# Optimization experiments

Hardware: AMD Instinct MI355X
Metric: run time of the kernel (lower is better)

Reference implementation:

```python
import jax, jax.numpy as jnp
import numpy as np

B, N, F_IN, T = 4, 512, 64, 16
K, F_CHEB, F_TIME, TS = 3, 64, 64, 1
E = 16384
LN_EPS = 1e-5


def setup_inputs() -> dict:
    key = jax.random.key(0)
    ks = jax.random.split(key, 18)
    s = 0.05
    X = jax.random.normal(ks[0], (B, N, F_IN, T), jnp.float32)
    # edges with guaranteed no self-loops (so remove_self_loops is a no-op)
    src = jax.random.randint(ks[1], (E,), 0, N, jnp.int32)
    off = jax.random.randint(ks[2], (E,), 1, N, jnp.int32)
    dst = (src + off) % N
    edge_index = jnp.stack([src, dst])
    return {
        'X': X,
        'edge_index': edge_index,
        'U1': jax.random.uniform(ks[3], (N,)) * s,
        'U2': jax.random.normal(ks[4], (F_IN, N)) * s,
        'U3': jax.random.uniform(ks[5], (F_IN,)) * s,
        'be': jax.random.normal(ks[6], (1, T, T)) * s,
        'Ve': jax.random.normal(ks[7], (T, T)) * s,
        'Ws1': jax.random.uniform(ks[8], (T,)) * s,
        'Ws2': jax.random.normal(ks[9], (F_IN, T)) * s,
        'Ws3': jax.random.uniform(ks[10], (F_IN,)) * s,
        'bs': jax.random.normal(ks[11], (1, N, N)) * s,
        'Vs': jax.random.normal(ks[12], (N, N)) * s,
        'W_cheb': jax.random.normal(ks[13], (K, F_IN, F_CHEB)) * s,
        'b_cheb': jax.random.uniform(ks[14], (F_CHEB,)) * s,
        'Wt': jax.random.normal(ks[15], (F_TIME, F_CHEB, 1, 3)) * s,
        'bt': jnp.zeros((F_TIME,), jnp.float32),
        'Wr': jax.random.normal(ks[16], (F_TIME, F_IN, 1, 1)) * s,
        'br': jnp.zeros((F_TIME,), jnp.float32),
        'gamma': jnp.ones((F_TIME,), jnp.float32),
        'beta': jnp.zeros((F_TIME,), jnp.float32),
    }


def _forward(edge_index, X, U1, U2, U3, be, Ve, Ws1, Ws2, Ws3, bs, Vs,
             W_cheb, b_cheb, Wt, bt, Wr, br, gamma, beta):
    Bn, Nn, Fn, Tn = X.shape
    # ---- temporal attention: (B,T,T)
    lhs_t = jnp.einsum('bnft,n->btf', X, U1) @ U2            # (B,T,N)
    rhs_t = jnp.einsum('f,bnft->bnt', U3, X)                 # (B,N,T)
    Et = jnp.matmul(Ve, jax.nn.sigmoid(jnp.matmul(lhs_t, rhs_t) + be))
    Et = jax.nn.softmax(Et, axis=1)
    # temporally re-weighted signal
    Xt = jnp.matmul(X.reshape(Bn, Nn * Fn, Tn), Et).reshape(Bn, Nn, Fn, Tn)
    # ---- spatial attention: (B,N,N)
    lhs_s = jnp.einsum('bnft,t->bnf', Xt, Ws1) @ Ws2         # (B,N,T)
    rhs_s = jnp.einsum('f,bnft->btn', Ws3, Xt)               # (B,T,N)
    S = jnp.matmul(Vs, jax.nn.sigmoid(jnp.matmul(lhs_s, rhs_s) + bs))
    S = jax.nn.softmax(S, axis=1)                            # (B,N,N)
    # ---- scaled sym-normalized Laplacian; lambda_max=2 so 2/lambda_max = 1.
    # edges: -D^-1/2 A D^-1/2 (E), +I self loops (N), then add_self_loops(-1) (N)
    row, col = edge_index[0], edge_index[1]
    ew = jnp.ones(row.shape, X.dtype)
    deg = jnp.zeros((Nn,), X.dtype).at[row].add(ew)
    dis = jnp.where(deg > 0, 1.0 / jnp.sqrt(jnp.maximum(deg, 1.0)), 0.0)  # deg is integral so max() only guards deg==0
    wn = -dis[row] * dis[col]
    loops = jnp.arange(Nn)
    rows = jnp.concatenate([row, loops, loops])
    cols = jnp.concatenate([col, loops, loops])
    norm = jnp.concatenate([wn, jnp.ones((Nn,), X.dtype), -jnp.ones((Nn,), X.dtype)])
    att_norm = norm[None, :] * S[:, rows, cols]              # (B,Etot)

    def prop(h, w):
        # propagate over transposed edges: gather at col, scatter-add at row
        # h: (B,T,N,F); w broadcastable to (B,1,Etot)
        msg = w[..., None] * h[:, :, cols, :]
        return jnp.zeros_like(h).at[:, :, rows, :].add(msg)

    xt = X.transpose(0, 3, 1, 2)                             # (B,T,N,F): ChebConv applied per timestep
    Tx0 = jnp.diagonal(S, axis1=1, axis2=2)[:, None, :, None] * xt  # diag(S) @ x
    out = jnp.einsum('btnf,fg->btng', Tx0, W_cheb[0])
    if W_cheb.shape[0] > 1:
        Tx1 = prop(Tx0, att_norm[:, None, :])
        out = out + jnp.einsum('btnf,fg->btng', Tx1, W_cheb[1])
    for k in range(2, W_cheb.shape[0]):
        Tx2 = 2.0 * prop(Tx1, norm[None, None, :]) - Tx0
        out = out + jnp.einsum('btnf,fg->btng', Tx2, W_cheb[k])
        Tx0, Tx1 = Tx1, Tx2
    X_hat = jax.nn.relu(out + b_cheb)                        # (B,T,N,Fc)
    # ---- time conv (1x3, stride (1,TS)) on (B,Fc,N,T) + residual 1x1 conv
    conv_t = jax.lax.conv_general_dilated(
        X_hat.transpose(0, 3, 2, 1), Wt, (1, TS), ((0, 0), (1, 1)),
        dimension_numbers=('NCHW', 'OIHW', 'NCHW')) + bt[None, :, None, None]
    conv_r = jax.lax.conv_general_dilated(
        X.transpose(0, 2, 1, 3), Wr, (1, TS), ((0, 0), (0, 0)),
        dimension_numbers=('NCHW', 'OIHW', 'NCHW')) + br[None, :, None, None]
    Z = jax.nn.relu(conv_r + conv_t).transpose(0, 3, 2, 1)   # (B,T,N,Ft)
    mu = jnp.mean(Z, -1, keepdims=True)
    var = jnp.var(Z, -1, keepdims=True)
    Z = (Z - mu) / jnp.sqrt(var + LN_EPS) * gamma + beta     # LayerNorm over Ft
    return Z.transpose(0, 2, 3, 1)                           # (B,N,Ft,T)


def reference(X, edge_index, U1, U2, U3, be, Ve, Ws1, Ws2, Ws3, bs, Vs,
              W_cheb, b_cheb, Wt, bt, Wr, br, gamma, beta):
    return _forward(edge_index, X, U1, U2, U3, be, Ve, Ws1, Ws2, Ws3, bs, Vs,
                    W_cheb, b_cheb, Wt, bt, Wr, br, gamma, beta)
```

## Files before the change

### kernel.cpp

```cpp
#include <hip/hip_runtime.h>
#include <math.h>

#define NB 4
#define NV 512
#define NF 64
#define NT 16
#define NE 16384

#define TX1_OFF    2097152u
#define TX2_OFF    4194304u
#define XHAT_OFF   6291456u
#define ST_OFF     TX1_OFF
#define SIGT_OFF   TX2_OFF
#define BST_OFF    8388608u
#define ET_OFF     8650752u
#define PART_OFF   8651776u
#define RHST_OFF   8684544u
#define LHSS_OFF   8717312u
#define RHSSN_OFF  8750080u
#define DIAGS_OFF  8782848u
#define WSATT_OFF  8784896u
#define CSRW_OFF   8850432u
#define WTT_OFF    8866816u
#define WRT_OFF    8879104u
#define DIS_OFF    8883200u
#define RHS3_OFF   8883712u
#define EW1_OFF    8916480u
#define FEND       8916544u

__global__ void k_hist(const int* __restrict__ row, int* __restrict__ counts) {
    __shared__ int h[512];
    int c = blockIdx.x, i = threadIdx.x;
    h[i] = 0; h[i + 256] = 0;
    __syncthreads();
    atomicAdd(&h[row[c * 256 + i]], 1);
    __syncthreads();
    counts[c * 512 + i] = h[i];
    counts[c * 512 + i + 256] = h[i + 256];
}

__global__ void k_scan2(int* __restrict__ counts, float* __restrict__ dis,
                        int* __restrict__ row_start) {
    __shared__ int sc[512];
    int r = threadIdx.x;
    int sum = 0;
    for (int c = 0; c < 64; ++c) {
        int v = counts[c * 512 + r];
        counts[c * 512 + r] = sum;
        sum += v;
    }
    dis[r] = sum > 0 ? 1.0f / sqrtf((float)sum) : 0.0f;
    sc[r] = sum;
    __syncthreads();
    for (int off = 1; off < 512; off <<= 1) {
        int v = sc[r];
        int add = (r >= off) ? sc[r - off] : 0;
        __syncthreads();
        sc[r] = v + add;
        __syncthreads();
    }
    int incl = sc[r];
    row_start[r] = incl - sum;
    if (r == 511) row_start[512] = incl;
}

__global__ void k_fill2(const int* __restrict__ ei, const int* __restrict__ counts,
                        const int* __restrict__ row_start, const float* __restrict__ dis,
                        int* __restrict__ csr_col, int* __restrict__ csr_row,
                        float* __restrict__ csr_w) {
    __shared__ int rowL[256];
    int c = blockIdx.x, i = threadIdx.x;
    int e = c * 256 + i;
    int r = ei[e];
    int col = ei[NE + e];
    rowL[i] = r;
    __syncthreads();
    int rank = 0;
    for (int j = 0; j < 256; ++j)
        if (j < i && rowL[j] == r) rank++;
    int pos = row_start[r] + counts[c * 512 + r] + rank;
    csr_col[pos] = col;
    csr_row[pos] = r;
    csr_w[pos] = -dis[r] * dis[col];
}

__global__ void k_wprep(const float* __restrict__ Wt, const float* __restrict__ Wr,
                        float* __restrict__ WtT, float* __restrict__ WrT) {
    int idx = blockIdx.x * 256 + threadIdx.x;
    if (idx < 12288) {
        int o = idx & 63, gd = idx >> 6;
        int g = gd / 3, dt = gd - g * 3;
        WtT[idx] = Wt[(o * 64 + g) * 3 + dt];
    } else if (idx < 16384) {
        int i2 = idx - 12288;
        int o = i2 & 63, f = i2 >> 6;
        WrT[i2] = Wr[o * 64 + f];
    }
}

__global__ void k_bst(const float* __restrict__ bs, float* __restrict__ bsT) {
    __shared__ float tile[64][65];
    int r0 = blockIdx.y * 64, c0 = blockIdx.x * 64;
    int c = threadIdx.x & 63, rq = threadIdx.x >> 6;
    for (int k = 0; k < 16; ++k) {
        int r = rq * 16 + k;
        tile[r][c] = bs[(r0 + r) * 512 + c0 + c];
    }
    __syncthreads();
    int r2 = threadIdx.x & 63;
    for (int k = 0; k < 16; ++k) {
        int c2 = rq * 16 + k;
        bsT[(size_t)(c0 + c2) * 512 + r0 + r2] = tile[r2][c2];
    }
}

__global__ void k_lhs1_partial(const float* __restrict__ X, const float* __restrict__ U1,
                               float* __restrict__ part) {
    int b = blockIdx.x >> 3, g = blockIdx.x & 7;
    int tid = threadIdx.x;
    float acc[4] = {0.f, 0.f, 0.f, 0.f};
    const float* Xb = X + (size_t)b * NV * 1024;
    int n0 = g * 64;
    for (int nn = 0; nn < 64; ++nn) {
        int n = n0 + nn;
        float u = U1[n];
        const float* xp = Xb + (size_t)n * 1024;
#pragma unroll
        for (int k = 0; k < 4; ++k) acc[k] += xp[tid + 256 * k] * u;
    }
#pragma unroll
    for (int k = 0; k < 4; ++k) part[(size_t)(b * 8 + g) * 1024 + tid + 256 * k] = acc[k];
}

__global__ void k_rhs_t(const float* __restrict__ X, const float* __restrict__ U3,
                        const float* __restrict__ Ws3,
                        float* __restrict__ rhs, float* __restrict__ rhs3) {
    int gid = blockIdx.x * 256 + threadIdx.x;
    int t = gid & 15, n = (gid >> 4) & 511, b = gid >> 13;
    const float* xp = X + ((size_t)(b * 512 + n)) * 1024 + t;
    float a = 0.f, a3 = 0.f;
#pragma unroll
    for (int f = 0; f < 64; ++f) {
        float v = xp[f * 16];
        a += U3[f] * v;
        a3 += Ws3[f] * v;
    }
    rhs[gid] = a;
    rhs3[gid] = a3;
}

__global__ void k_temporal(const float* __restrict__ part, const float* __restrict__ rhs_g,
                           const float* __restrict__ U2, const float* __restrict__ be,
                           const float* __restrict__ Ve, const float* __restrict__ Ws1,
                           float* __restrict__ Et, float* __restrict__ ew1) {
    __shared__ float lhs1[1024];
    __shared__ float rhsL[8192];
    __shared__ float M[1024];
    __shared__ float Esig[256];
    __shared__ float Et0[256];
    __shared__ float red[32];
    __shared__ float EtL[256];
    int b = blockIdx.x, tid = threadIdx.x;
#pragma unroll
    for (int k = 0; k < 4; ++k) {
        int idx = tid + 256 * k;
        float s = 0.f;
        for (int g = 0; g < 8; ++g) s += part[(size_t)(b * 8 + g) * 1024 + idx];
        lhs1[idx] = s;
    }
    for (int k = 0; k < 32; ++k) rhsL[tid + 256 * k] = rhs_g[(size_t)b * 8192 + tid + 256 * k];
    __syncthreads();
    {
        float acc[4] = {0.f, 0.f, 0.f, 0.f};
        int fA[4], tA[4];
#pragma unroll
        for (int k = 0; k < 4; ++k) { int idx = tid + 256 * k; fA[k] = idx >> 4; tA[k] = idx & 15; }
        for (int n = 0; n < 512; ++n) {
#pragma unroll
            for (int k = 0; k < 4; ++k) acc[k] += U2[fA[k] * 512 + n] * rhsL[n * 16 + tA[k]];
        }
#pragma unroll
        for (int k = 0; k < 4; ++k) M[tid + 256 * k] = acc[k];
    }
    __syncthreads();
    {
        int t1 = tid >> 4, t2 = tid & 15;
        float s = 0.f;
        for (int f = 0; f < 64; ++f) s += lhs1[f * 16 + t1] * M[f * 16 + t2];
        s += be[t1 * 16 + t2];
        Esig[tid] = 1.f / (1.f + expf(-s));
    }
    __syncthreads();
    {
        int t1 = tid >> 4, t2 = tid & 15;
        float s = 0.f;
        for (int k = 0; k < 16; ++k) s += Ve[t1 * 16 + k] * Esig[k * 16 + t2];
        Et0[tid] = s;
    }
    __syncthreads();
    if (tid < 16) {
        float m = -1e30f;
        for (int k = 0; k < 16; ++k) m = fmaxf(m, Et0[k * 16 + tid]);
        float s = 0.f;
        for (int k = 0; k < 16; ++k) s += expf(Et0[k * 16 + tid] - m);
        red[tid] = m; red[16 + tid] = 1.f / s;
    }
    __syncthreads();
    {
        int t2 = tid & 15;
        float etv = expf(Et0[tid] - red[t2]) * red[16 + t2];
        Et[b * 256 + tid] = etv;
        EtL[tid] = etv;
    }
    __syncthreads();
    if (tid < 16) {
        float s = 0.f;
        for (int t = 0; t < 16; ++t) s += EtL[tid * 16 + t] * Ws1[t];
        ew1[b * 16 + tid] = s;
    }
}

__global__ __launch_bounds__(256) void k_spat2(const float* __restrict__ X,
                                               const float* __restrict__ ew1,
                                               const float* __restrict__ rhs3,
                                               const float* __restrict__ Et,
                                               const float* __restrict__ Ws2,
                                               float* __restrict__ lhs_s,
                                               float* __restrict__ rhs_sn) {
    int wv = threadIdx.x >> 6, lane = threadIdx.x & 63;
    int bn = blockIdx.x * 4 + wv;
    int b = bn >> 9;
    const float4* xp = (const float4*)(X + (size_t)bn * 1024 + lane * 16);
    float4 x0 = xp[0], x1 = xp[1], x2 = xp[2], x3 = xp[3];
    const float* e1 = ew1 + b * 16;
    float l1 = x0.x * e1[0] + x0.y * e1[1] + x0.z * e1[2] + x0.w * e1[3]
             + x1.x * e1[4] + x1.y * e1[5] + x1.z * e1[6] + x1.w * e1[7]
             + x2.x * e1[8] + x2.y * e1[9] + x2.z * e1[10] + x2.w * e1[11]
             + x3.x * e1[12] + x3.y * e1[13] + x3.z * e1[14] + x3.w * e1[15];
    const float4* wp = (const float4*)(Ws2 + lane * 16);
    float4 w0 = wp[0], w1 = wp[1], w2 = wp[2], w3 = wp[3];
    float p[16] = {l1 * w0.x, l1 * w0.y, l1 * w0.z, l1 * w0.w,
                   l1 * w1.x, l1 * w1.y, l1 * w1.z, l1 * w1.w,
                   l1 * w2.x, l1 * w2.y, l1 * w2.z, l1 * w2.w,
                   l1 * w3.x, l1 * w3.y, l1 * w3.z, l1 * w3.w};
#pragma unroll
    for (int off = 32; off; off >>= 1) {
#pragma unroll
        for (int k = 0; k < 16; ++k) p[k] += __shfl_xor(p[k], off);
    }
    if (lane == 0) {
        float4* lp = (float4*)(lhs_s + (size_t)bn * 16);
        lp[0] = make_float4(p[0], p[1], p[2], p[3]);
        lp[1] = make_float4(p[4], p[5], p[6], p[7]);
        lp[2] = make_float4(p[8], p[9], p[10], p[11]);
        lp[3] = make_float4(p[12], p[13], p[14], p[15]);
    }
    if (lane < 16) {
        const float* r3 = rhs3 + (size_t)bn * 16;
        const float* Eb = Et + b * 256;
        float s = 0.f;
#pragma unroll
        for (int tp = 0; tp < 16; ++tp) s += r3[tp] * Eb[tp * 16 + lane];
        rhs_sn[(size_t)bn * 16 + lane] = s;
    }
}

__global__ void k_sigT(const float* __restrict__ lhs_s, const float* __restrict__ rhs_sn,
                       const float* __restrict__ bsT, float* __restrict__ sigT) {
    int gid = blockIdx.x * 256 + threadIdx.x;
    int k = gid & 511, j = (gid >> 9) & 511, b = gid >> 18;
    const float4* lp = (const float4*)(lhs_s + (size_t)(b * 512 + k) * 16);
    const float4* rp = (const float4*)(rhs_sn + (size_t)(b * 512 + j) * 16);
    float s = 0.f;
#pragma unroll
    for (int q = 0; q < 4; ++q) {
        float4 a = lp[q], c = rp[q];
        s += a.x * c.x + a.y * c.y + a.z * c.z + a.w * c.w;
    }
    s += bsT[(size_t)j * 512 + k];
    sigT[gid] = 1.f / (1.f + expf(-s));
}

__global__ __launch_bounds__(256) void k_gemm_s(const float* __restrict__ sigT,
                                                const float* __restrict__ Vs,
                                                float* __restrict__ S0T) {
    __shared__ float As[32 * 68];
    __shared__ float Bs[32 * 68];
    int bI = blockIdx.x, bJ = blockIdx.y, b = blockIdx.z;
    int tid = threadIdx.x, tx = tid & 15, ty = tid >> 4;
    float acc[4][4] = {};
    const float* Ab = sigT + ((size_t)b * 512 + bJ * 64) * 512;
    const float* Bb = Vs + (size_t)bI * 64 * 512;
    for (int k0 = 0; k0 < 512; k0 += 32) {
#pragma unroll
        for (int p = 0; p < 2; ++p) {
            int idx = tid + 256 * p;
            int row = idx >> 3, kk = (idx & 7) * 4;
            float4 a = *(const float4*)(Ab + (size_t)row * 512 + k0 + kk);
            As[(kk + 0) * 68 + row] = a.x; As[(kk + 1) * 68 + row] = a.y;
            As[(kk + 2) * 68 + row] = a.z; As[(kk + 3) * 68 + row] = a.w;
            float4 v = *(const float4*)(Bb + (size_t)row * 512 + k0 + kk);
            Bs[(kk + 0) * 68 + row] = v.x; Bs[(kk + 1) * 68 + row] = v.y;
            Bs[(kk + 2) * 68 + row] = v.z; Bs[(kk + 3) * 68 + row] = v.w;
        }
        __syncthreads();
#pragma unroll
        for (int kk = 0; kk < 32; ++kk) {
            float4 a = *(const float4*)(As + kk * 68 + ty * 4);
            float4 bv = *(const float4*)(Bs + kk * 68 + tx * 4);
            acc[0][0] += a.x * bv.x; acc[0][1] += a.x * bv.y; acc[0][2] += a.x * bv.z; acc[0][3] += a.x * bv.w;
            acc[1][0] += a.y * bv.x; acc[1][1] += a.y * bv.y; acc[1][2] += a.y * bv.z; acc[1][3] += a.y * bv.w;
            acc[2][0] += a.z * bv.x; acc[2][1] += a.z * bv.y; acc[2][2] += a.z * bv.z; acc[2][3] += a.z * bv.w;
            acc[3][0] += a.w * bv.x; acc[3][1] += a.w * bv.y; acc[3][2] += a.w * bv.z; acc[3][3] += a.w * bv.w;
        }
        __syncthreads();
    }
    float* Cb = S0T + ((size_t)b * 512 + bJ * 64) * 512 + bI * 64;
#pragma unroll
    for (int y = 0; y < 4; ++y) {
        int j = ty * 4 + y;
        *(float4*)(Cb + (size_t)j * 512 + tx * 4) =
            make_float4(acc[y][0], acc[y][1], acc[y][2], acc[y][3]);
    }
}

__global__ void k_softmax_s(float* __restrict__ ST, float* __restrict__ diagS) {
    __shared__ float red[4];
    int bj = blockIdx.x;
    int b = bj >> 9, j = bj & 511;
    float* row = ST + (size_t)bj * 512;
    int tid = threadIdx.x;
    float v0 = row[tid], v1 = row[tid + 256];
    float m = fmaxf(v0, v1);
    for (int off = 32; off; off >>= 1) m = fmaxf(m, __shfl_xor(m, off));
    if ((tid & 63) == 0) red[tid >> 6] = m;
    __syncthreads();
    m = fmaxf(fmaxf(red[0], red[1]), fmaxf(red[2], red[3]));
    __syncthreads();
    float e0 = expf(v0 - m), e1 = expf(v1 - m);
    float s = e0 + e1;
    for (int off = 32; off; off >>= 1) s += __shfl_xor(s, off);
    if ((tid & 63) == 0) red[tid >> 6] = s;
    __syncthreads();
    s = red[0] + red[1] + red[2] + red[3];
    float inv = 1.f / s;
    float r0 = e0 * inv, r1 = e1 * inv;
    row[tid] = r0;
    row[tid + 256] = r1;
    if (j < 256) { if (tid == j) diagS[b * 512 + j] = r0; }
    else { if (tid == j - 256) diagS[b * 512 + j] = r1; }
}

__global__ void k_wS(const int* __restrict__ csr_col, const int* __restrict__ csr_row,
                     const float* __restrict__ csr_w, const float* __restrict__ ST,
                     const float* __restrict__ diagS, float* __restrict__ wS) {
    int gid = blockIdx.x * 256 + threadIdx.x;
    int pos = gid & (NE - 1), b = gid >> 14;
    int c = csr_col[pos], r = csr_row[pos];
    wS[gid] = csr_w[pos] * ST[((size_t)(b * 512 + c)) * 512 + r] * diagS[b * 512 + c];
}

__global__ __launch_bounds__(256) void k_prop1(const float* __restrict__ X,
                                               const float* __restrict__ wS,
                                               const int* __restrict__ csr_col,
                                               const int* __restrict__ row_start,
                                               float* __restrict__ Tx1) {
    int blk = ((blockIdx.x & 7) << 8) + (blockIdx.x >> 3);
    int b = blk >> 9, i = blk & 511;
    int tid = threadIdx.x;
    int s = row_start[i], e2 = row_start[i + 1];
    const float4* Xb = (const float4*)(X + (size_t)b * 512 * 1024);
    const float* wb = wS + (size_t)b * NE;
    float4 acc = make_float4(0.f, 0.f, 0.f, 0.f);
    for (int p = s; p < e2; ++p) {
        int col = csr_col[p];
        float w = wb[p];
        float4 v = Xb[col * 256 + tid];
        acc.x += w * v.x; acc.y += w * v.y; acc.z += w * v.z; acc.w += w * v.w;
    }
    *(float4*)(Tx1 + (size_t)blk * 1024 + tid * 4) = acc;
}

__global__ __launch_bounds__(256) void k_prop2(const float* __restrict__ Tx1,
                                               const float* __restrict__ X,
                                               const float* __restrict__ diagS,
                                               const float* __restrict__ csr_w,
                                               const int* __restrict__ csr_col,
                                               const int* __restrict__ row_start,
                                               float* __restrict__ Tx2) {
    int blk = ((blockIdx.x & 7) << 8) + (blockIdx.x >> 3);
    int b = blk >> 9, i = blk & 511;
    int tid = threadIdx.x;
    int s = row_start[i], e2 = row_start[i + 1];
    const float4* T1b = (const float4*)(Tx1 + (size_t)b * 512 * 1024);
    float4 acc = make_float4(0.f, 0.f, 0.f, 0.f);
    for (int p = s; p < e2; ++p) {
        int col = csr_col[p];
        float w = csr_w[p];
        float4 v = T1b[col * 256 + tid];
        acc.x += w * v.x; acc.y += w * v.y; acc.z += w * v.z; acc.w += w * v.w;
    }
    float ds = diagS[blk];
    float4 x0 = *(const float4*)(X + (size_t)blk * 1024 + tid * 4);
    float4 o;
    o.x = 2.f * acc.x - ds * x0.x;
    o.y = 2.f * acc.y - ds * x0.y;
    o.z = 2.f * acc.z - ds * x0.z;
    o.w = 2.f * acc.w - ds * x0.w;
    *(float4*)(Tx2 + (size_t)blk * 1024 + tid * 4) = o;
}

__global__ __launch_bounds__(256) void k_cheb(const float* __restrict__ X,
                                              const float* __restrict__ Tx1,
                                              const float* __restrict__ Tx2,
                                              const float* __restrict__ diagS,
                                              const float* __restrict__ Wc,
                                              const float* __restrict__ bc,
                                              float* __restrict__ Xh) {
    __shared__ float t0s[4][1024], t1s[4][1024], t2s[4][1024];
    int bn0 = blockIdx.x * 4;
    int tid = threadIdx.x;
    int r = tid >> 6, l = tid & 63;
    int bn = bn0 + r;
    float ds = diagS[bn];
    const float4* xp = (const float4*)(X + (size_t)bn * 1024);
    const float4* p1 = (const float4*)(Tx1 + (size_t)bn * 1024);
    const float4* p2 = (const float4*)(Tx2 + (size_t)bn * 1024);
#pragma unroll
    for (int k = 0; k < 4; ++k) {
        float4 v = xp[k * 64 + l];
        v.x *= ds; v.y *= ds; v.z *= ds; v.w *= ds;
        ((float4*)t0s[r])[k * 64 + l] = v;
        ((float4*)t1s[r])[k * 64 + l] = p1[k * 64 + l];
        ((float4*)t2s[r])[k * 64 + l] = p2[k * 64 + l];
    }
    __syncthreads();
    int g4 = (l & 15) * 4, t4 = (l >> 4) * 4;
    float4 bv = *(const float4*)(bc + g4);
    float4 acc0 = make_float4(bv.x, bv.x, bv.x, bv.x);
    float4 acc1 = make_float4(bv.y, bv.y, bv.y, bv.y);
    float4 acc2 = make_float4(bv.z, bv.z, bv.z, bv.z);
    float4 acc3 = make_float4(bv.w, bv.w, bv.w, bv.w);
    const float* t0r = t0s[r];
    const float* t1r = t1s[r];
    const float* t2r = t2s[r];
    for (int f = 0; f < 64; ++f) {
        float4 a0 = *(const float4*)(t0r + f * 16 + t4);
        float4 a1 = *(const float4*)(t1r + f * 16 + t4);
        float4 a2 = *(const float4*)(t2r + f * 16 + t4);
        float4 w0 = *(const float4*)(Wc + f * 64 + g4);
        float4 w1 = *(const float4*)(Wc + 4096 + f * 64 + g4);
        float4 w2 = *(const float4*)(Wc + 8192 + f * 64 + g4);
        acc0.x += w0.x * a0.x + w1.x * a1.x + w2.x * a2.x;
        acc0.y += w0.x * a0.y + w1.x * a1.y + w2.x * a2.y;
        acc0.z += w0.x * a0.z + w1.x * a1.z + w2.x * a2.z;
        acc0.w += w0.x * a0.w + w1.x * a1.w + w2.x * a2.w;
        acc1.x += w0.y * a0.x + w1.y * a1.x + w2.y * a2.x;
        acc1.y += w0.y * a0.y + w1.y * a1.y + w2.y * a2.y;
        acc1.z += w0.y * a0.z + w1.y * a1.z + w2.y * a2.z;
        acc1.w += w0.y * a0.w + w1.y * a1.w + w2.y * a2.w;
        acc2.x += w0.z * a0.x + w1.z * a1.x + w2.z * a2.x;
        acc2.y += w0.z * a0.y + w1.z * a1.y + w2.z * a2.y;
        acc2.z += w0.z * a0.z + w1.z * a1.z + w2.z * a2.z;
        acc2.w += w0.z * a0.w + w1.z * a1.w + w2.z * a2.w;
        acc3.x += w0.w * a0.x + w1.w * a1.x + w2.w * a2.x;
        acc3.y += w0.w * a0.y + w1.w * a1.y + w2.w * a2.y;
        acc3.z += w0.w * a0.z + w1.w * a1.z + w2.w * a2.z;
        acc3.w += w0.w * a0.w + w1.w * a1.w + w2.w * a2.w;
    }
    float* op = Xh + (size_t)bn * 1024;
    float4 o0, o1, o2, o3;
    o0.x = fmaxf(acc0.x, 0.f); o0.y = fmaxf(acc0.y, 0.f); o0.z = fmaxf(acc0.z, 0.f); o0.w = fmaxf(acc0.w, 0.f);
    o1.x = fmaxf(acc1.x, 0.f); o1.y = fmaxf(acc1.y, 0.f); o1.z = fmaxf(acc1.z, 0.f); o1.w = fmaxf(acc1.w, 0.f);
    o2.x = fmaxf(acc2.x, 0.f); o2.y = fmaxf(acc2.y, 0.f); o2.z = fmaxf(acc2.z, 0.f); o2.w = fmaxf(acc2.w, 0.f);
    o3.x = fmaxf(acc3.x, 0.f); o3.y = fmaxf(acc3.y, 0.f); o3.z = fmaxf(acc3.z, 0.f); o3.w = fmaxf(acc3.w, 0.f);
    *(float4*)(op + (g4 + 0) * 16 + t4) = o0;
    *(float4*)(op + (g4 + 1) * 16 + t4) = o1;
    *(float4*)(op + (g4 + 2) * 16 + t4) = o2;
    *(float4*)(op + (g4 + 3) * 16 + t4) = o3;
}

__global__ __launch_bounds__(256) void k_out(const float* __restrict__ X,
                                             const float* __restrict__ Xh,
                                             const float* __restrict__ WtT,
                                             const float* __restrict__ WrT,
                                             const float* __restrict__ bt,
                                             const float* __restrict__ br,
                                             const float* __restrict__ gamma,
                                             const float* __restrict__ beta,
                                             float* __restrict__ out) {
    __shared__ float xh[64 * 20];
    __shared__ float xl[64 * 16];
    __shared__ float red[4160];
    int bn = blockIdx.x;
    int tid = threadIdx.x;
    int o = tid & 63, q = tid >> 6;
    {
        int g = tid & 63, s4 = tid >> 6;
        int slot = (s4 == 0) ? 0 : 16 + s4;
        xh[g * 20 + slot] = 0.f;
    }
    {
        float4 v = ((const float4*)(Xh + (size_t)bn * 1024))[tid];
        int g = tid >> 2, t0 = (tid & 3) * 4;
        xh[g * 20 + t0 + 1] = v.x;
        xh[g * 20 + t0 + 2] = v.y;
        xh[g * 20 + t0 + 3] = v.z;
        xh[g * 20 + t0 + 4] = v.w;
        float4 u = ((const float4*)(X + (size_t)bn * 1024))[tid];
        *(float4*)(xl + tid * 4) = u;
    }
    __syncthreads();
    float acc[16];
#pragma unroll
    for (int k = 0; k < 16; ++k) acc[k] = 0.f;
    for (int gi = 0; gi < 16; ++gi) {
        int g = q * 16 + gi;
        const float4* xp = (const float4*)(xh + g * 20);
        float4 xa = xp[0], xb = xp[1], xc = xp[2], xd = xp[3], xe = xp[4];
        float xs[20] = {xa.x, xa.y, xa.z, xa.w, xb.x, xb.y, xb.z, xb.w,
                        xc.x, xc.y, xc.z, xc.w, xd.x, xd.y, xd.z, xd.w,
                        xe.x, xe.y, xe.z, xe.w};
        float w0 = WtT[(g * 3 + 0) * 64 + o];
        float w1 = WtT[(g * 3 + 1) * 64 + o];
        float w2 = WtT[(g * 3 + 2) * 64 + o];
#pragma unroll
        for (int tt = 0; tt < 16; ++tt)
            acc[tt] += xs[tt] * w0 + xs[tt + 1] * w1 + xs[tt + 2] * w2;
    }
    for (int fi = 0; fi < 16; ++fi) {
        int f = q * 16 + fi;
        const float4* xp = (const float4*)(xl + f * 16);
        float4 xa = xp[0], xb = xp[1], xc = xp[2], xd = xp[3];
        float xs[16] = {xa.x, xa.y, xa.z, xa.w, xb.x, xb.y, xb.z, xb.w,
                        xc.x, xc.y, xc.z, xc.w, xd.x, xd.y, xd.z, xd.w};
        float w = WrT[f * 64 + o];
#pragma unroll
        for (int tt = 0; tt < 16; ++tt) acc[tt] += xs[tt] * w;
    }
#pragma unroll
    for (int tt = 0; tt < 16; ++tt) red[q * 1024 + tt * 64 + o] = acc[tt];
    __syncthreads();
    float bsum = bt[o] + br[o];
    float go = gamma[o], bo = beta[o];
    float zv4[4];
#pragma unroll
    for (int tt = 0; tt < 4; ++tt) {
        int t = q * 4 + tt;
        float s = bsum;
#pragma unroll
        for (int qq = 0; qq < 4; ++qq) s += red[qq * 1024 + t * 64 + o];
        zv4[tt] = fmaxf(s, 0.f);
    }
    __syncthreads();
#pragma unroll
    for (int tt = 0; tt < 4; ++tt) {
        int t = q * 4 + tt;
        float zv = zv4[tt];
        float s = zv, sq = zv * zv;
        for (int off = 32; off; off >>= 1) {
            s += __shfl_xor(s, off);
            sq += __shfl_xor(sq, off);
        }
        float mu = s * (1.f / 64.f);
        float var = sq * (1.f / 64.f) - mu * mu;
        red[t * 65 + o] = (zv - mu) * rsqrtf(var + 1e-5f) * go + bo;
    }
    __syncthreads();
#pragma unroll
    for (int k = 0; k < 4; ++k) {
        int i = tid + 256 * k;
        out[(size_t)bn * 1024 + i] = red[(i & 15) * 65 + (i >> 4)];
    }
}

extern "C" void kernel_launch(void* const* d_in, const int* in_sizes, int n_in,
                              void* d_out, int out_size, void* d_ws, size_t ws_size,
                              hipStream_t stream) {
    const float* X     = (const float*)d_in[0];
    const int*   ei    = (const int*)d_in[1];
    const float* U1    = (const float*)d_in[2];
    const float* U2    = (const float*)d_in[3];
    const float* U3    = (const float*)d_in[4];
    const float* be    = (const float*)d_in[5];
    const float* Ve    = (const float*)d_in[6];
    const float* Ws1   = (const float*)d_in[7];
    const float* Ws2   = (const float*)d_in[8];
    const float* Ws3   = (const float*)d_in[9];
    const float* bs    = (const float*)d_in[10];
    const float* Vs    = (const float*)d_in[11];
    const float* Wc    = (const float*)d_in[12];
    const float* bc    = (const float*)d_in[13];
    const float* Wt    = (const float*)d_in[14];
    const float* bt    = (const float*)d_in[15];
    const float* Wr    = (const float*)d_in[16];
    const float* br    = (const float*)d_in[17];
    const float* gamma = (const float*)d_in[18];
    const float* beta  = (const float*)d_in[19];

    float* ws = (float*)d_ws;
    float* Tx1    = ws + TX1_OFF;
    float* Tx2    = ws + TX2_OFF;
    float* Xh     = ws + XHAT_OFF;
    float* ST     = ws + ST_OFF;
    float* sigT   = ws + SIGT_OFF;
    float* bsT    = ws + BST_OFF;
    float* Et     = ws + ET_OFF;
    float* part   = ws + PART_OFF;
    float* rhs_t  = ws + RHST_OFF;
    float* lhs_s  = ws + LHSS_OFF;
    float* rhs_sn = ws + RHSSN_OFF;
    float* diagS  = ws + DIAGS_OFF;
    float* wS     = ws + WSATT_OFF;
    float* csr_w  = ws + CSRW_OFF;
    float* WtT    = ws + WTT_OFF;
    float* WrT    = ws + WRT_OFF;
    float* dis    = ws + DIS_OFF;
    float* rhs3   = ws + RHS3_OFF;
    float* ew1    = ws + EW1_OFF;

    int* ib        = (int*)(ws + FEND);
    int* row_start = ib;
    int* csr_col   = ib + 516;
    int* csr_row   = csr_col + NE;
    int* counts    = csr_row + NE;

    k_hist<<<64, 256, 0, stream>>>(ei, counts);
    k_scan2<<<1, 512, 0, stream>>>(counts, dis, row_start);
    k_fill2<<<64, 256, 0, stream>>>(ei, counts, row_start, dis, csr_col, csr_row, csr_w);

    k_wprep<<<64, 256, 0, stream>>>(Wt, Wr, WtT, WrT);
    k_bst<<<dim3(8, 8), 256, 0, stream>>>(bs, bsT);

    k_lhs1_partial<<<32, 256, 0, stream>>>(X, U1, part);
    k_rhs_t<<<128, 256, 0, stream>>>(X, U3, Ws3, rhs_t, rhs3);
    k_temporal<<<4, 256, 0, stream>>>(part, rhs_t, U2, be, Ve, Ws1, Et, ew1);

    k_spat2<<<512, 256, 0, stream>>>(X, ew1, rhs3, Et, Ws2, lhs_s, rhs_sn);
    k_sigT<<<4096, 256, 0, stream>>>(lhs_s, rhs_sn, bsT, sigT);
    k_gemm_s<<<dim3(8, 8, 4), 256, 0, stream>>>(sigT, Vs, ST);
    k_softmax_s<<<2048, 256, 0, stream>>>(ST, diagS);
    k_wS<<<256, 256, 0, stream>>>(csr_col, csr_row, csr_w, ST, diagS, wS);

    k_prop1<<<2048, 256, 0, stream>>>(X, wS, csr_col, row_start, Tx1);
    k_prop2<<<2048, 256, 0, stream>>>(Tx1, X, diagS, csr_w, csr_col, row_start, Tx2);
    k_cheb<<<512, 256, 0, stream>>>(X, Tx1, Tx2, diagS, Wc, bc, Xh);

    k_out<<<2048, 256, 0, stream>>>(X, Xh, WtT, WrT, bt, br, gamma, beta, (float*)d_out);
}
```

Before: 177.5 us.

## Merge small prep kernels and split sparse propagation rows across wavefronts

The two weight/bias transpose kernels become one launch, and the lhs/rhs temporal input reductions over X become another, cutting launch count. The Chebyshev propagation kernels now give each wavefront its own graph row and a quarter of the feature slice, instead of all four wavefronts of a block handling one row. This spreads per-row CSR walks across more independent waves, which is meant to improve memory-level parallelism and balance over uneven row degrees. The per-thread gathered bytes per edge stay the same, and each row's index list is now read by four blocks.

```diff
diff --git a/kernel.cpp b/kernel.cpp
--- a/kernel.cpp
+++ b/kernel.cpp
@@ -84,69 +84,73 @@
     csr_w[pos] = -dis[r] * dis[col];
 }
 
-__global__ void k_wprep(const float* __restrict__ Wt, const float* __restrict__ Wr,
-                        float* __restrict__ WtT, float* __restrict__ WrT) {
-    int idx = blockIdx.x * 256 + threadIdx.x;
-    if (idx < 12288) {
-        int o = idx & 63, gd = idx >> 6;
-        int g = gd / 3, dt = gd - g * 3;
-        WtT[idx] = Wt[(o * 64 + g) * 3 + dt];
-    } else if (idx < 16384) {
-        int i2 = idx - 12288;
-        int o = i2 & 63, f = i2 >> 6;
-        WrT[i2] = Wr[o * 64 + f];
-    }
-}
-
-__global__ void k_bst(const float* __restrict__ bs, float* __restrict__ bsT) {
+__global__ void k_wtrans(const float* __restrict__ Wt, const float* __restrict__ Wr,
+                         const float* __restrict__ bs,
+                         float* __restrict__ WtT, float* __restrict__ WrT,
+                         float* __restrict__ bsT) {
     __shared__ float tile[64][65];
-    int r0 = blockIdx.y * 64, c0 = blockIdx.x * 64;
-    int c = threadIdx.x & 63, rq = threadIdx.x >> 6;
-    for (int k = 0; k < 16; ++k) {
-        int r = rq * 16 + k;
-        tile[r][c] = bs[(r0 + r) * 512 + c0 + c];
-    }
-    __syncthreads();
-    int r2 = threadIdx.x & 63;
-    for (int k = 0; k < 16; ++k) {
-        int c2 = rq * 16 + k;
-        bsT[(size_t)(c0 + c2) * 512 + r0 + r2] = tile[r2][c2];
-    }
-}
-
-__global__ void k_lhs1_partial(const float* __restrict__ X, const float* __restrict__ U1,
-                               float* __restrict__ part) {
-    int b = blockIdx.x >> 3, g = blockIdx.x & 7;
+    int bid = blockIdx.x;
+    if (bid < 64) {
+        int r0 = (bid >> 3) * 64, c0 = (bid & 7) * 64;
+        int c = threadIdx.x & 63, rq = threadIdx.x >> 6;
+        for (int k = 0; k < 16; ++k) {
+            int r = rq * 16 + k;
+            tile[r][c] = bs[(r0 + r) * 512 + c0 + c];
+        }
+        __syncthreads();
+        int r2 = threadIdx.x & 63;
+        for (int k = 0; k < 16; ++k) {
+            int c2 = rq * 16 + k;
+            bsT[(size_t)(c0 + c2) * 512 + r0 + r2] = tile[r2][c2];
+        }
+    } else {
+        int idx = (bid - 64) * 256 + threadIdx.x;
+        if (idx < 12288) {
+            int o = idx & 63, gd = idx >> 6;
+            int g = gd / 3, dt = gd - g * 3;
+            WtT[idx] = Wt[(o * 64 + g) * 3 + dt];
+        } else if (idx < 16384) {
+            int i2 = idx - 12288;
+            int o = i2 & 63, f = i2 >> 6;
+            WrT[i2] = Wr[o * 64 + f];
+        }
+    }
+}
+
+__global__ void k_xin(const float* __restrict__ X, const float* __restrict__ U1,
+                      const float* __restrict__ U3, const float* __restrict__ Ws3,
+                      float* __restrict__ part, float* __restrict__ rhs,
+                      float* __restrict__ rhs3) {
+    int bid = blockIdx.x;
     int tid = threadIdx.x;
-    float acc[4] = {0.f, 0.f, 0.f, 0.f};
-    const float* Xb = X + (size_t)b * NV * 1024;
-    int n0 = g * 64;
-    for (int nn = 0; nn < 64; ++nn) {
-        int n = n0 + nn;
-        float u = U1[n];
-        const float* xp = Xb + (size_t)n * 1024;
-#pragma unroll
-        for (int k = 0; k < 4; ++k) acc[k] += xp[tid + 256 * k] * u;
-    }
-#pragma unroll
-    for (int k = 0; k < 4; ++k) part[(size_t)(b * 8 + g) * 1024 + tid + 256 * k] = acc[k];
-}
-
-__global__ void k_rhs_t(const float* __restrict__ X, const float* __restrict__ U3,
-                        const float* __restrict__ Ws3,
-                        float* __restrict__ rhs, float* __restrict__ rhs3) {
-    int gid = blockIdx.x * 256 + threadIdx.x;
-    int t = gid & 15, n = (gid >> 4) & 511, b = gid >> 13;
-    const float* xp = X + ((size_t)(b * 512 + n)) * 1024 + t;
-    float a = 0.f, a3 = 0.f;
-#pragma unroll
-    for (int f = 0; f < 64; ++f) {
-        float v = xp[f * 16];
-        a += U3[f] * v;
-        a3 += Ws3[f] * v;
-    }
-    rhs[gid] = a;
-    rhs3[gid] = a3;
+    if (bid < 32) {
+        int b = bid >> 3, g = bid & 7;
+        float acc[4] = {0.f, 0.f, 0.f, 0.f};
+        const float* Xb = X + (size_t)b * NV * 1024;
+        int n0 = g * 64;
+        for (int nn = 0; nn < 64; ++nn) {
+            int n = n0 + nn;
+            float u = U1[n];
+            const float* xp = Xb + (size_t)n * 1024;
+#pragma unroll
+            for (int k = 0; k < 4; ++k) acc[k] += xp[tid + 256 * k] * u;
+        }
+#pragma unroll
+        for (int k = 0; k < 4; ++k) part[(size_t)(b * 8 + g) * 1024 + tid + 256 * k] = acc[k];
+    } else {
+        int gid = (bid - 32) * 256 + tid;
+        int t = gid & 15;
+        const float* xp = X + ((size_t)(gid >> 4)) * 1024 + t;
+        float a = 0.f, a3 = 0.f;
+#pragma unroll
+        for (int f = 0; f < 64; ++f) {
+            float v = xp[f * 16];
+            a += U3[f] * v;
+            a3 += Ws3[f] * v;
+        }
+        rhs[gid] = a;
+        rhs3[gid] = a3;
+    }
 }
 
 __global__ void k_temporal(const float* __restrict__ part, const float* __restrict__ rhs_g,
@@ -365,20 +369,21 @@
                                                const int* __restrict__ csr_col,
                                                const int* __restrict__ row_start,
                                                float* __restrict__ Tx1) {
-    int blk = ((blockIdx.x & 7) << 8) + (blockIdx.x >> 3);
-    int b = blk >> 9, i = blk & 511;
-    int tid = threadIdx.x;
+    int logical = ((blockIdx.x & 7) << 8) + (blockIdx.x >> 3);
+    int b = logical >> 9, tile = (logical >> 7) & 3, rq = logical & 127;
+    int w = threadIdx.x >> 6, lane = threadIdx.x & 63;
+    int i = rq * 4 + w;
     int s = row_start[i], e2 = row_start[i + 1];
-    const float4* Xb = (const float4*)(X + (size_t)b * 512 * 1024);
+    const float* Xb = X + (size_t)b * 512 * 1024 + tile * 256 + lane * 4;
     const float* wb = wS + (size_t)b * NE;
     float4 acc = make_float4(0.f, 0.f, 0.f, 0.f);
     for (int p = s; p < e2; ++p) {
         int col = csr_col[p];
-        float w = wb[p];
-        float4 v = Xb[col * 256 + tid];
-        acc.x += w * v.x; acc.y += w * v.y; acc.z += w * v.z; acc.w += w * v.w;
-    }
-    *(float4*)(Tx1 + (size_t)blk * 1024 + tid * 4) = acc;
+        float wv = wb[p];
+        float4 v = *(const float4*)(Xb + (size_t)col * 1024);
+        acc.x += wv * v.x; acc.y += wv * v.y; acc.z += wv * v.z; acc.w += wv * v.w;
+    }
+    *(float4*)(Tx1 + ((size_t)(b * 512 + i)) * 1024 + tile * 256 + lane * 4) = acc;
 }
 
 __global__ __launch_bounds__(256) void k_prop2(const float* __restrict__ Tx1,
@@ -388,26 +393,28 @@
                                                const int* __restrict__ csr_col,
                                                const int* __restrict__ row_start,
                                                float* __restrict__ Tx2) {
-    int blk = ((blockIdx.x & 7) << 8) + (blockIdx.x >> 3);
-    int b = blk >> 9, i = blk & 511;
-    int tid = threadIdx.x;
+    int logical = ((blockIdx.x & 7) << 8) + (blockIdx.x >> 3);
+    int b = logical >> 9, tile = (logical >> 7) & 3, rq = logical & 127;
+    int w = threadIdx.x >> 6, lane = threadIdx.x & 63;
+    int i = rq * 4 + w;
     int s = row_start[i], e2 = row_start[i + 1];
-    const float4* T1b = (const float4*)(Tx1 + (size_t)b * 512 * 1024);
+    const float* T1b = Tx1 + (size_t)b * 512 * 1024 + tile * 256 + lane * 4;
     float4 acc = make_float4(0.f, 0.f, 0.f, 0.f);
     for (int p = s; p < e2; ++p) {
         int col = csr_col[p];
-        float w = csr_w[p];
-        float4 v = T1b[col * 256 + tid];
-        acc.x += w * v.x; acc.y += w * v.y; acc.z += w * v.z; acc.w += w * v.w;
-    }
-    float ds = diagS[blk];
-    float4 x0 = *(const float4*)(X + (size_t)blk * 1024 + tid * 4);
+        float wv = csr_w[p];
+        float4 v = *(const float4*)(T1b + (size_t)col * 1024);
+        acc.x += wv * v.x; acc.y += wv * v.y; acc.z += wv * v.z; acc.w += wv * v.w;
+    }
+    float ds = diagS[b * 512 + i];
+    size_t off = ((size_t)(b * 512 + i)) * 1024 + tile * 256 + lane * 4;
+    float4 x0 = *(const float4*)(X + off);
     float4 o;
     o.x = 2.f * acc.x - ds * x0.x;
     o.y = 2.f * acc.y - ds * x0.y;
     o.z = 2.f * acc.z - ds * x0.z;
     o.w = 2.f * acc.w - ds * x0.w;
-    *(float4*)(Tx2 + (size_t)blk * 1024 + tid * 4) = o;
+    *(float4*)(Tx2 + off) = o;
 }
 
 __global__ __launch_bounds__(256) void k_cheb(const float* __restrict__ X,
@@ -629,11 +636,9 @@
     k_scan2<<<1, 512, 0, stream>>>(counts, dis, row_start);
     k_fill2<<<64, 256, 0, stream>>>(ei, counts, row_start, dis, csr_col, csr_row, csr_w);
 
-    k_wprep<<<64, 256, 0, stream>>>(Wt, Wr, WtT, WrT);
-    k_bst<<<dim3(8, 8), 256, 0, stream>>>(bs, bsT);
-
-    k_lhs1_partial<<<32, 256, 0, stream>>>(X, U1, part);
-    k_rhs_t<<<128, 256, 0, stream>>>(X, U3, Ws3, rhs_t, rhs3);
+    k_wtrans<<<128, 256, 0, stream>>>(Wt, Wr, bs, WtT, WrT, bsT);
+
+    k_xin<<<160, 256, 0, stream>>>(X, U1, U3, Ws3, part, rhs_t, rhs3);
     k_temporal<<<4, 256, 0, stream>>>(part, rhs_t, U2, be, Ve, Ws1, Et, ew1);
 
     k_spat2<<<512, 256, 0, stream>>>(X, ew1, rhs3, Et, Ws2, lhs_s, rhs_sn);
```

Result: slower. 181.2 us (+2.1%).

## Merge prep kernels into one launch and split temporal U2 GEMM across blocks

Applied to the files above, without the earlier changes.

Merges the histogram, bs transpose, weight transposes, lhs partial and rhs_t kernels into one block-indexed launch, so five launches become one. Moves the U2·rhs product out of the 4-block temporal kernel into a new 32-block partial kernel whose partial sums are reduced in k_temporal. This is meant to cut launch overhead and the long serial 512-iteration loop on only four blocks. The cost is one extra launch, a small partial buffer and heterogeneous blocks within the merged kernel.

```diff
diff --git a/kernel.cpp b/kernel.cpp
--- a/kernel.cpp
+++ b/kernel.cpp
@@ -26,17 +26,85 @@
 #define DIS_OFF    8883200u
 #define RHS3_OFF   8883712u
 #define EW1_OFF    8916480u
-#define FEND       8916544u
-
-__global__ void k_hist(const int* __restrict__ row, int* __restrict__ counts) {
+#define MPART_OFF  8916544u
+#define FEND       8949312u
+
+__global__ void k_prep(const int* __restrict__ ei, int* __restrict__ counts,
+                       const float* __restrict__ Wt, const float* __restrict__ Wr,
+                       const float* __restrict__ bs,
+                       float* __restrict__ WtT, float* __restrict__ WrT,
+                       float* __restrict__ bsT,
+                       const float* __restrict__ X, const float* __restrict__ U1,
+                       const float* __restrict__ U3, const float* __restrict__ Ws3,
+                       float* __restrict__ part, float* __restrict__ rhs,
+                       float* __restrict__ rhs3) {
     __shared__ int h[512];
-    int c = blockIdx.x, i = threadIdx.x;
-    h[i] = 0; h[i + 256] = 0;
-    __syncthreads();
-    atomicAdd(&h[row[c * 256 + i]], 1);
-    __syncthreads();
-    counts[c * 512 + i] = h[i];
-    counts[c * 512 + i + 256] = h[i + 256];
+    __shared__ float tile[64][65];
+    int bid = blockIdx.x, tid = threadIdx.x;
+    if (bid < 64) {
+        int c = bid;
+        h[tid] = 0; h[tid + 256] = 0;
+        __syncthreads();
+        atomicAdd(&h[ei[c * 256 + tid]], 1);
+        __syncthreads();
+        counts[c * 512 + tid] = h[tid];
+        counts[c * 512 + tid + 256] = h[tid + 256];
+    } else if (bid < 128) {
+        int tb = bid - 64;
+        int r0 = (tb >> 3) * 64, c0 = (tb & 7) * 64;
+        int c = tid & 63, rq = tid >> 6;
+        for (int k = 0; k < 16; ++k) {
+            int r = rq * 16 + k;
+            tile[r][c] = bs[(r0 + r) * 512 + c0 + c];
+        }
+        __syncthreads();
+        int r2 = tid & 63;
+        for (int k = 0; k < 16; ++k) {
+            int c2 = rq * 16 + k;
+            bsT[(size_t)(c0 + c2) * 512 + r0 + r2] = tile[r2][c2];
+        }
+    } else if (bid < 192) {
+        int idx = (bid - 128) * 256 + tid;
+        if (idx < 12288) {
+            int o = idx & 63, gd = idx >> 6;
+            int g = gd / 3, dt = gd - g * 3;
+            WtT[idx] = Wt[(o * 64 + g) * 3 + dt];
+        } else {
+            int i2 = idx - 12288;
+            int o = i2 & 63, f = i2 >> 6;
+            WrT[i2] = Wr[o * 64 + f];
+        }
+    } else {
+        int sub = bid - 192;
+        if (sub < 32) {
+            int b = sub >> 3, g = sub & 7;
+            float acc[4] = {0.f, 0.f, 0.f, 0.f};
+            const float* Xb = X + (size_t)b * NV * 1024;
+            int n0 = g * 64;
+            for (int nn = 0; nn < 64; ++nn) {
+                int n = n0 + nn;
+                float u = U1[n];
+                const float* xp = Xb + (size_t)n * 1024;
+#pragma unroll
+                for (int k = 0; k < 4; ++k) acc[k] += xp[tid + 256 * k] * u;
+            }
+#pragma unroll
+            for (int k = 0; k < 4; ++k) part[(size_t)(b * 8 + g) * 1024 + tid + 256 * k] = acc[k];
+        } else {
+            int gid = (sub - 32) * 256 + tid;
+            int t = gid & 15;
+            const float* xp = X + ((size_t)(gid >> 4)) * 1024 + t;
+            float a = 0.f, a3 = 0.f;
+#pragma unroll
+            for (int f = 0; f < 64; ++f) {
+                float v = xp[f * 16];
+                a += U3[f] * v;
+                a3 += Ws3[f] * v;
+            }
+            rhs[gid] = a;
+            rhs3[gid] = a3;
+        }
+    }
 }
 
 __global__ void k_scan2(int* __restrict__ counts, float* __restrict__ dis,
@@ -84,77 +152,34 @@
     csr_w[pos] = -dis[r] * dis[col];
 }
 
-__global__ void k_wprep(const float* __restrict__ Wt, const float* __restrict__ Wr,
-                        float* __restrict__ WtT, float* __restrict__ WrT) {
-    int idx = blockIdx.x * 256 + threadIdx.x;
-    if (idx < 12288) {
-        int o = idx & 63, gd = idx >> 6;
-        int g = gd / 3, dt = gd - g * 3;
-        WtT[idx] = Wt[(o * 64 + g) * 3 + dt];
-    } else if (idx < 16384) {
-        int i2 = idx - 12288;
-        int o = i2 & 63, f = i2 >> 6;
-        WrT[i2] = Wr[o * 64 + f];
-    }
-}
-
-__global__ void k_bst(const float* __restrict__ bs, float* __restrict__ bsT) {
-    __shared__ float tile[64][65];
-    int r0 = blockIdx.y * 64, c0 = blockIdx.x * 64;
-    int c = threadIdx.x & 63, rq = threadIdx.x >> 6;
-    for (int k = 0; k < 16; ++k) {
-        int r = rq * 16 + k;
-        tile[r][c] = bs[(r0 + r) * 512 + c0 + c];
-    }
-    __syncthreads();
-    int r2 = threadIdx.x & 63;
-    for (int k = 0; k < 16; ++k) {
-        int c2 = rq * 16 + k;
-        bsT[(size_t)(c0 + c2) * 512 + r0 + r2] = tile[r2][c2];
-    }
-}
-
-__global__ void k_lhs1_partial(const float* __restrict__ X, const float* __restrict__ U1,
-                               float* __restrict__ part) {
+__global__ void k_mpart(const float* __restrict__ rhs_g, const float* __restrict__ U2,
+                        float* __restrict__ Mpart) {
+    __shared__ float rhsL[1024];
     int b = blockIdx.x >> 3, g = blockIdx.x & 7;
     int tid = threadIdx.x;
+#pragma unroll
+    for (int k = 0; k < 4; ++k)
+        rhsL[tid + 256 * k] = rhs_g[(size_t)b * 8192 + g * 1024 + tid + 256 * k];
+    __syncthreads();
     float acc[4] = {0.f, 0.f, 0.f, 0.f};
-    const float* Xb = X + (size_t)b * NV * 1024;
+    int fA[4], tA[4];
+#pragma unroll
+    for (int k = 0; k < 4; ++k) { int idx = tid + 256 * k; fA[k] = idx >> 4; tA[k] = idx & 15; }
     int n0 = g * 64;
     for (int nn = 0; nn < 64; ++nn) {
-        int n = n0 + nn;
-        float u = U1[n];
-        const float* xp = Xb + (size_t)n * 1024;
-#pragma unroll
-        for (int k = 0; k < 4; ++k) acc[k] += xp[tid + 256 * k] * u;
-    }
-#pragma unroll
-    for (int k = 0; k < 4; ++k) part[(size_t)(b * 8 + g) * 1024 + tid + 256 * k] = acc[k];
-}
-
-__global__ void k_rhs_t(const float* __restrict__ X, const float* __restrict__ U3,
-                        const float* __restrict__ Ws3,
-                        float* __restrict__ rhs, float* __restrict__ rhs3) {
-    int gid = blockIdx.x * 256 + threadIdx.x;
-    int t = gid & 15, n = (gid >> 4) & 511, b = gid >> 13;
-    const float* xp = X + ((size_t)(b * 512 + n)) * 1024 + t;
-    float a = 0.f, a3 = 0.f;
-#pragma unroll
-    for (int f = 0; f < 64; ++f) {
-        float v = xp[f * 16];
-        a += U3[f] * v;
-        a3 += Ws3[f] * v;
-    }
-    rhs[gid] = a;
-    rhs3[gid] = a3;
-}
-
-__global__ void k_temporal(const float* __restrict__ part, const float* __restrict__ rhs_g,
-                           const float* __restrict__ U2, const float* __restrict__ be,
+#pragma unroll
+        for (int k = 0; k < 4; ++k)
+            acc[k] += U2[fA[k] * 512 + n0 + nn] * rhsL[nn * 16 + tA[k]];
+    }
+#pragma unroll
+    for (int k = 0; k < 4; ++k) Mpart[(size_t)(b * 8 + g) * 1024 + tid + 256 * k] = acc[k];
+}
+
+__global__ void k_temporal(const float* __restrict__ part, const float* __restrict__ Mpart,
+                           const float* __restrict__ be,
                            const float* __restrict__ Ve, const float* __restrict__ Ws1,
                            float* __restrict__ Et, float* __restrict__ ew1) {
     __shared__ float lhs1[1024];
-    __shared__ float rhsL[8192];
     __shared__ float M[1024];
     __shared__ float Esig[256];
     __shared__ float Et0[256];
@@ -164,23 +189,13 @@
 #pragma unroll
     for (int k = 0; k < 4; ++k) {
         int idx = tid + 256 * k;
-        float s = 0.f;
-        for (int g = 0; g < 8; ++g) s += part[(size_t)(b * 8 + g) * 1024 + idx];
+        float s = 0.f, m = 0.f;
+        for (int g = 0; g < 8; ++g) {
+            s += part[(size_t)(b * 8 + g) * 1024 + idx];
+            m += Mpart[(size_t)(b * 8 + g) * 1024 + idx];
+        }
         lhs1[idx] = s;
-    }
-    for (int k = 0; k < 32; ++k) rhsL[tid + 256 * k] = rhs_g[(size_t)b * 8192 + tid + 256 * k];
-    __syncthreads();
-    {
-        float acc[4] = {0.f, 0.f, 0.f, 0.f};
-        int fA[4], tA[4];
-#pragma unroll
-        for (int k = 0; k < 4; ++k) { int idx = tid + 256 * k; fA[k] = idx >> 4; tA[k] = idx & 15; }
-        for (int n = 0; n < 512; ++n) {
-#pragma unroll
-            for (int k = 0; k < 4; ++k) acc[k] += U2[fA[k] * 512 + n] * rhsL[n * 16 + tA[k]];
-        }
-#pragma unroll
-        for (int k = 0; k < 4; ++k) M[tid + 256 * k] = acc[k];
+        M[idx] = m;
     }
     __syncthreads();
     {
@@ -618,6 +633,7 @@
     float* dis    = ws + DIS_OFF;
     float* rhs3   = ws + RHS3_OFF;
     float* ew1    = ws + EW1_OFF;
+    float* Mpart  = ws + MPART_OFF;
 
     int* ib        = (int*)(ws + FEND);
     int* row_start = ib;
@@ -625,16 +641,13 @@
     int* csr_row   = csr_col + NE;
     int* counts    = csr_row + NE;
 
-    k_hist<<<64, 256, 0, stream>>>(ei, counts);
+    k_prep<<<352, 256, 0, stream>>>(ei, counts, Wt, Wr, bs, WtT, WrT, bsT,
+                                    X, U1, U3, Ws3, part, rhs_t, rhs3);
     k_scan2<<<1, 512, 0, stream>>>(counts, dis, row_start);
     k_fill2<<<64, 256, 0, stream>>>(ei, counts, row_start, dis, csr_col, csr_row, csr_w);
 
-    k_wprep<<<64, 256, 0, stream>>>(Wt, Wr, WtT, WrT);
-    k_bst<<<dim3(8, 8), 256, 0, stream>>>(bs, bsT);
-
-    k_lhs1_partial<<<32, 256, 0, stream>>>(X, U1, part);
-    k_rhs_t<<<128, 256, 0, stream>>>(X, U3, Ws3, rhs_t, rhs3);
-    k_temporal<<<4, 256, 0, stream>>>(part, rhs_t, U2, be, Ve, Ws1, Et, ew1);
+    k_mpart<<<32, 256, 0, stream>>>(rhs_t, U2, Mpart);
+    k_temporal<<<4, 256, 0, stream>>>(part, Mpart, be, Ve, Ws1, Et, ew1);
 
     k_spat2<<<512, 256, 0, stream>>>(X, ew1, rhs3, Et, Ws2, lhs_s, rhs_sn);
     k_sigT<<<4096, 256, 0, stream>>>(lhs_s, rhs_sn, bsT, sigT);
```

Measured after the change: 163.5 us. 1.09x faster.
